# Optimization experiments

Measured on AMD Instinct MI355X. Metric: run time of the kernel, lower is better.

Reference implementation:

```python
import jax, jax.numpy as jnp
import numpy as np

N, IN_F, HID, HEADS, OUT = 50000, 128, 32, 4, 40
E = 800000
LN_EPS = 1e-5


def setup_inputs() -> dict:
    key = jax.random.key(0)
    ks = jax.random.split(key, 16)
    d1 = HEADS * HID  # 128
    s_in = 1.0 / np.sqrt(IN_F)
    s_d1 = 1.0 / np.sqrt(d1)
    return {
        "x": jax.random.normal(ks[0], (N, IN_F), jnp.float32),
        "edge_index": jax.random.randint(ks[1], (2, E), 0, N, jnp.int64),
        # layer 1 (GATv2, heads=4, concat=True)
        "Wl1": jax.random.normal(ks[2], (IN_F, d1), jnp.float32) * s_in,
        "bl1": jnp.zeros((d1,), jnp.float32),
        "Wr1": jax.random.normal(ks[3], (IN_F, d1), jnp.float32) * s_in,
        "br1": jnp.zeros((d1,), jnp.float32),
        "att1": jax.random.normal(ks[4], (HEADS, HID), jnp.float32) * s_d1,
        "b1": jnp.zeros((d1,), jnp.float32),
        # LayerNorm over hidden_channels*heads
        "g1": jnp.ones((d1,), jnp.float32),
        "be1": jnp.zeros((d1,), jnp.float32),
        # layer 2 (GATv2, heads=1, concat=False)
        "Wl2": jax.random.normal(ks[5], (d1, OUT), jnp.float32) * s_d1,
        "bl2": jnp.zeros((OUT,), jnp.float32),
        "Wr2": jax.random.normal(ks[6], (d1, OUT), jnp.float32) * s_d1,
        "br2": jnp.zeros((OUT,), jnp.float32),
        "att2": jax.random.normal(ks[7], (1, OUT), jnp.float32) / np.sqrt(OUT),
        "b2": jnp.zeros((OUT,), jnp.float32),
    }


def gatv2(x, src, tgt, Wl, bl, Wr, br, att, bias, heads, C, concat):
    n = x.shape[0]
    xl = (x @ Wl + bl).reshape(n, heads, C)  # source transform
    xr = (x @ Wr + br).reshape(n, heads, C)  # target transform
    h = xl[src] + xr[tgt]                    # [E,H,C]
    e = jnp.sum(jax.nn.leaky_relu(h, 0.2) * att, axis=-1)  # [E,H]
    # segment softmax over edges sharing the same target node
    m = jax.ops.segment_max(e, tgt, num_segments=n)        # [N,H]
    m = jnp.where(jnp.isfinite(m), m, 0.0)
    p = jnp.exp(e - m[tgt])
    s = jax.ops.segment_sum(p, tgt, num_segments=n)
    alpha = p / (s[tgt] + 1e-16)                           # [E,H]
    out = jax.ops.segment_sum(alpha[..., None] * xl[src], tgt, num_segments=n)  # [N,H,C]
    out = out.reshape(n, heads * C) if concat else out.mean(axis=1)
    return out + bias


def layer_norm(x, g, b):
    mu = x.mean(-1, keepdims=True)
    var = x.var(-1, keepdims=True)
    return (x - mu) * jax.lax.rsqrt(var + LN_EPS) * g + b


def reference(x, edge_index, Wl1, bl1, Wr1, br1, att1, b1, g1, be1,
              Wl2, bl2, Wr2, br2, att2, b2):
    src, tgt = edge_index[0], edge_index[1]
    h = gatv2(x, src, tgt, Wl1, bl1, Wr1, br1, att1, b1, HEADS, HID, True)
    h = jax.nn.elu(layer_norm(h, g1, be1))
    # dropout is identity in eval mode
    return gatv2(h, src, tgt, Wl2, bl2, Wr2, br2, att2, b2, 1, OUT, False)
```

## Files before the change

### kernel.cpp

```cpp
#include <hip/hip_runtime.h>
#include <hip/hip_bf16.h>
#include <math.h>

#define NN 50000
#define EE 800000
#define NB_SCAN 49

typedef __attribute__((ext_vector_type(8))) short bf16x8;
typedef __attribute__((ext_vector_type(4))) float f32x4;
typedef __attribute__((ext_vector_type(2))) float f32x2;
typedef __attribute__((ext_vector_type(8))) unsigned short ushortx8;

#define OFF_XBF  ((size_t)0)
#define SZ_XBF   ((size_t)NN * 128 * 2)
#define OFF_XL1B (OFF_XBF + SZ_XBF)
#define SZ_XL1B  ((size_t)NN * 128 * 2)
#define OFF_XR1  (OFF_XL1B + SZ_XL1B)
#define SZ_XR1   ((size_t)NN * 128 * 4)
#define OFF_H1B  (OFF_XR1 + SZ_XR1)
#define SZ_H1B   ((size_t)NN * 128 * 2)
#define OFF_XL2B (OFF_H1B + SZ_H1B)
#define SZ_XL2B  ((size_t)NN * 40 * 2)
#define OFF_XR2  (OFF_XL2B + SZ_XL2B)
#define SZ_XR2   ((size_t)NN * 40 * 4)
#define OFF_BP1  (OFF_XR2 + SZ_XR2)
#define SZ_BP1   ((size_t)32768 * 2)
#define OFF_BP2  (OFF_BP1 + SZ_BP1)
#define SZ_BP2   ((size_t)10240 * 2)
#define OFF_BB1  (OFF_BP2 + SZ_BP2)
#define SZ_BB1   ((size_t)1024)
#define OFF_BB2  (OFF_BB1 + SZ_BB1)
#define SZ_BB2   ((size_t)512)
#define OFF_DEG  (OFF_BB2 + SZ_BB2)
#define SZ_DEG   ((size_t)NN * 4)
#define OFF_OFFS (OFF_DEG + SZ_DEG)
#define SZ_OFFS  ((size_t)200192)
#define OFF_CUR  (OFF_OFFS + SZ_OFFS)
#define SZ_CUR   ((size_t)NN * 4)
#define OFF_CSR  (OFF_CUR + SZ_CUR)
#define SZ_CSR   ((size_t)EE * 4)
#define OFF_BSUM (OFF_CSR + SZ_CSR)
#define SZ_BSUM  ((size_t)256)

__device__ __forceinline__ unsigned short f2bf(float f) {
    union { float f; unsigned u; } v;
    v.f = f;
    unsigned r = v.u + 0x7fffu + ((v.u >> 16) & 1u);
    return (unsigned short)(r >> 16);
}
__device__ __forceinline__ f32x2 bf2f2(unsigned u) {
    union { unsigned u; float f; } lo, hi;
    lo.u = u << 16;
    hi.u = u & 0xffff0000u;
    f32x2 r;
    r.x = lo.f;
    r.y = hi.f;
    return r;
}

__device__ __forceinline__ f32x2 pk_add(f32x2 a, f32x2 b) {
    f32x2 d;
    asm("v_pk_add_f32 %0, %1, %2" : "=v"(d) : "v"(a), "v"(b));
    return d;
}
__device__ __forceinline__ f32x2 pk_mul(f32x2 a, f32x2 b) {
    f32x2 d;
    asm("v_pk_mul_f32 %0, %1, %2" : "=v"(d) : "v"(a), "v"(b));
    return d;
}
__device__ __forceinline__ f32x2 pk_fma(f32x2 a, f32x2 b, f32x2 c) {
    f32x2 d;
    asm("v_pk_fma_f32 %0, %1, %2, %3" : "=v"(d) : "v"(a), "v"(b), "v"(c));
    return d;
}
__device__ __forceinline__ f32x2 pk_abs2(f32x2 a) {
    f32x2 r;
    r.x = __builtin_fabsf(a.x);
    r.y = __builtin_fabsf(a.y);
    return r;
}

#define DPP_ADD(t, ctrl) \
    ((t) + __int_as_float(__builtin_amdgcn_mov_dpp(__float_as_int(t), (ctrl), 0xF, 0xF, true)))

__global__ void prep_kernel(
    const float* __restrict__ x, unsigned short* __restrict__ XBF,
    const float* __restrict__ Wl1, const float* __restrict__ bl1,
    const float* __restrict__ Wr1, const float* __restrict__ br1,
    const float* __restrict__ Wl2, const float* __restrict__ bl2,
    const float* __restrict__ Wr2, const float* __restrict__ br2,
    unsigned short* __restrict__ BP1, float* __restrict__ BB1,
    unsigned short* __restrict__ BP2, float* __restrict__ BB2,
    int* __restrict__ DEG) {
    int i = blockIdx.x * blockDim.x + threadIdx.x;
    if (i < NN * 128 / 8) {
        const float4* p = (const float4*)x + (size_t)i * 2;
        float4 v0 = p[0], v1 = p[1];
        ushortx8 o;
        o[0] = f2bf(v0.x); o[1] = f2bf(v0.y); o[2] = f2bf(v0.z); o[3] = f2bf(v0.w);
        o[4] = f2bf(v1.x); o[5] = f2bf(v1.y); o[6] = f2bf(v1.z); o[7] = f2bf(v1.w);
        *((ushortx8*)XBF + i) = o;
    }
    if (i < NN) DEG[i] = 0;
    if (i < 32768) {
        int j = i & 7, l = (i >> 3) & 63, nt = (i >> 9) & 15, kt = i >> 13;
        int k = kt * 32 + ((l >> 4) << 3) + j;
        int n = nt * 16 + (l & 15);
        float v = (n < 128) ? Wl1[k * 128 + n] : Wr1[k * 128 + (n - 128)];
        BP1[i] = f2bf(v);
    }
    if (i < 10240) {
        int j = i & 7, l = (i >> 3) & 63;
        int rest = i >> 9;
        int nt = rest % 5, kt = rest / 5;
        int k = kt * 32 + ((l >> 4) << 3) + j;
        int n = nt * 16 + (l & 15);
        float v = (n < 40) ? Wl2[k * 40 + n] : Wr2[k * 40 + (n - 40)];
        BP2[i] = f2bf(v);
    }
    if (i < 256) BB1[i] = (i < 128) ? bl1[i] : br1[i - 128];
    if (i < 80) BB2[i] = (i < 40) ? bl2[i] : br2[i - 40];
}

__global__ void hist_kernel(const int* __restrict__ tgts, int* __restrict__ deg, int e_) {
    int e = blockIdx.x * blockDim.x + threadIdx.x;
    if (e < e_) atomicAdd(&deg[tgts[e]], 1);
}

__global__ __launch_bounds__(1024) void scan_bsum_kernel(
    const int* __restrict__ deg, int* __restrict__ bsum, int n) {
    __shared__ int ws[16];
    int lane = threadIdx.x & 63, w = threadIdx.x >> 6;
    int i = blockIdx.x * 1024 + threadIdx.x;
    int v = (i < n) ? deg[i] : 0;
#pragma unroll
    for (int d = 32; d >= 1; d >>= 1) v += __shfl_xor(v, d, 64);
    if (lane == 0) ws[w] = v;
    __syncthreads();
    if (threadIdx.x < 16) {
        int xv = ws[threadIdx.x];
#pragma unroll
        for (int d = 8; d >= 1; d >>= 1) xv += __shfl_xor(xv, d, 16);
        if (threadIdx.x == 0) bsum[blockIdx.x] = xv;
    }
}

__global__ __launch_bounds__(1024) void scan_final_kernel(
    const int* __restrict__ deg, const int* __restrict__ bsum,
    int* __restrict__ off, int* __restrict__ cur, int n) {
    __shared__ int wsum[16];
    __shared__ int carrySh;
    int lane = threadIdx.x & 63, w = threadIdx.x >> 6;
    if (threadIdx.x < 64) {
        int v = ((int)threadIdx.x < (int)blockIdx.x) ? bsum[threadIdx.x] : 0;
#pragma unroll
        for (int d = 32; d >= 1; d >>= 1) v += __shfl_xor(v, d, 64);
        if (threadIdx.x == 0) carrySh = v;
    }
    int i = blockIdx.x * 1024 + threadIdx.x;
    int v = (i < n) ? deg[i] : 0;
    int incl = v;
#pragma unroll
    for (int d = 1; d < 64; d <<= 1) {
        int t = __shfl_up(incl, d, 64);
        if (lane >= d) incl += t;
    }
    if (lane == 63) wsum[w] = incl;
    __syncthreads();
    if (threadIdx.x < 16) {
        int xv = wsum[threadIdx.x];
#pragma unroll
        for (int d = 1; d < 16; d <<= 1) {
            int t = __shfl_up(xv, d, 16);
            if ((int)threadIdx.x >= d) xv += t;
        }
        wsum[threadIdx.x] = xv;
    }
    __syncthreads();
    int add = (w > 0) ? wsum[w - 1] : 0;
    int carry = carrySh;
    if (i < n) {
        int tot = carry + incl + add;
        off[i + 1] = tot;
        cur[i] = tot - v;
    }
    if (i == 0) off[0] = 0;
}

__global__ void scatter_kernel(const int* __restrict__ srcs, const int* __restrict__ tgts,
                               int* __restrict__ cur, int* __restrict__ csr, int e_) {
    int e = blockIdx.x * blockDim.x + threadIdx.x;
    if (e < e_) {
        int t = tgts[e];
        int pos = atomicAdd(&cur[t], 1);
        csr[pos] = srcs[e];
    }
}

__global__ __launch_bounds__(256) void gemm_mfma_kernel(
    const unsigned short* __restrict__ Abf, const unsigned short* __restrict__ BP,
    const float* __restrict__ bias, unsigned short* __restrict__ Cbf,
    float* __restrict__ Cf, int M, int NT, int NSPLIT) {
    int wave = (blockIdx.x * blockDim.x + threadIdx.x) >> 6;
    int lane = threadIdx.x & 63;
    int r0 = wave * 16;
    if (r0 >= M) return;
    int koff = (lane >> 4) << 3;
    const unsigned short* ap = &Abf[(size_t)(r0 + (lane & 15)) * 128 + koff];
    bf16x8 a0 = *(const bf16x8*)(ap);
    bf16x8 a1 = *(const bf16x8*)(ap + 32);
    bf16x8 a2 = *(const bf16x8*)(ap + 64);
    bf16x8 a3 = *(const bf16x8*)(ap + 96);
    int NR = (NT << 4) - NSPLIT;
    int col = lane & 15;
    int rb = r0 + ((lane >> 4) << 2);
    size_t ktStride = (size_t)NT * 512;
    for (int nt = 0; nt < NT; ++nt) {
        const unsigned short* bp = &BP[((size_t)nt * 64 + lane) * 8];
        f32x4 acc = {0.f, 0.f, 0.f, 0.f};
        acc = __builtin_amdgcn_mfma_f32_16x16x32_bf16(a0, *(const bf16x8*)(bp), acc, 0, 0, 0);
        acc = __builtin_amdgcn_mfma_f32_16x16x32_bf16(a1, *(const bf16x8*)(bp + ktStride), acc, 0, 0, 0);
        acc = __builtin_amdgcn_mfma_f32_16x16x32_bf16(a2, *(const bf16x8*)(bp + 2 * ktStride), acc, 0, 0, 0);
        acc = __builtin_amdgcn_mfma_f32_16x16x32_bf16(a3, *(const bf16x8*)(bp + 3 * ktStride), acc, 0, 0, 0);
        int c = (nt << 4) + col;
        float bb = bias[c];
        if (c < NSPLIT) {
#pragma unroll
            for (int j = 0; j < 4; ++j) Cbf[(size_t)(rb + j) * NSPLIT + c] = f2bf(acc[j] + bb);
        } else {
#pragma unroll
            for (int j = 0; j < 4; ++j) Cf[(size_t)(rb + j) * NR + (c - NSPLIT)] = acc[j] + bb;
        }
    }
}

__global__ __launch_bounds__(256) void gat_edge1_kernel(
    const unsigned short* __restrict__ XL1B, const float* __restrict__ XR1,
    const int* __restrict__ off, const int* __restrict__ csr,
    const float* __restrict__ att, const float* __restrict__ b1,
    const float* __restrict__ g1, const float* __restrict__ be1,
    unsigned short* __restrict__ H1B) {
    int wid = threadIdx.x >> 6;
    int lane = threadIdx.x & 63;
    int node = blockIdx.x * 4 + wid;
    if (node >= NN) return;
    int grp = lane >> 4;
    int sub = lane & 15;
    int cbase = sub << 3;
    const float* xrrow = &XR1[(size_t)node * 128];
    float4 xrA = *(const float4*)&xrrow[cbase];
    float4 xrB = *(const float4*)&xrrow[cbase + 4];
    float4 atA = *(const float4*)&att[cbase];
    float4 atB = *(const float4*)&att[cbase + 4];
    f32x2 xr01 = {xrA.x, xrA.y}, xr23 = {xrA.z, xrA.w};
    f32x2 xr45 = {xrB.x, xrB.y}, xr67 = {xrB.z, xrB.w};
    f32x2 at01 = {atA.x, atA.y}, at23 = {atA.z, atA.w};
    f32x2 at45 = {atB.x, atB.y}, at67 = {atB.z, atB.w};
    f32x2 c06 = {0.6f, 0.6f}, c04 = {0.4f, 0.4f};
    f32x2 acc01 = {0.f, 0.f}, acc23 = {0.f, 0.f}, acc45 = {0.f, 0.f}, acc67 = {0.f, 0.f};
    float s = 0.f;
    int jb = off[node], je = off[node + 1];
    int deg = je - jb;

    auto process = [&](uint4 q, int eo) {
        f32x2 xl01 = bf2f2(q.x), xl23 = bf2f2(q.y), xl45 = bf2f2(q.z), xl67 = bf2f2(q.w);
        f32x2 h01 = pk_add(xl01, xr01);
        f32x2 h23 = pk_add(xl23, xr23);
        f32x2 h45 = pk_add(xl45, xr45);
        f32x2 h67 = pk_add(xl67, xr67);
        f32x2 u01 = pk_fma(pk_abs2(h01), c04, pk_mul(h01, c06));
        f32x2 u23 = pk_fma(pk_abs2(h23), c04, pk_mul(h23, c06));
        f32x2 u45 = pk_fma(pk_abs2(h45), c04, pk_mul(h45, c06));
        f32x2 u67 = pk_fma(pk_abs2(h67), c04, pk_mul(h67, c06));
        f32x2 t2 = pk_mul(u01, at01);
        t2 = pk_fma(u23, at23, t2);
        t2 = pk_fma(u45, at45, t2);
        t2 = pk_fma(u67, at67, t2);
        float t = t2.x + t2.y;
        t = DPP_ADD(t, 0xB1);
        t = DPP_ADD(t, 0x4E);
        t = (eo < deg) ? t : -1e30f;
        float p = __expf(t);
        f32x2 pp;
        pp.x = p;
        pp.y = p;
        acc01 = pk_fma(pp, xl01, acc01);
        acc23 = pk_fma(pp, xl23, acc23);
        acc45 = pk_fma(pp, xl45, acc45);
        acc67 = pk_fma(pp, xl67, acc67);
        s += p;
    };

    for (int ch = 0; ch < deg; ch += 16) {
        int sidx = csr[min(jb + ch + sub, je - 1)];
        int s0 = __shfl(sidx, grp, 16);
        int s1 = __shfl(sidx, 4 + grp, 16);
        int s2 = __shfl(sidx, 8 + grp, 16);
        int s3 = __shfl(sidx, 12 + grp, 16);
        uint4 q0 = *(const uint4*)&XL1B[(size_t)s0 * 128 + cbase];
        uint4 q1 = *(const uint4*)&XL1B[(size_t)s1 * 128 + cbase];
        uint4 q2 = *(const uint4*)&XL1B[(size_t)s2 * 128 + cbase];
        uint4 q3 = *(const uint4*)&XL1B[(size_t)s3 * 128 + cbase];
        process(q0, ch + grp);
        process(q1, ch + 4 + grp);
        process(q2, ch + 8 + grp);
        process(q3, ch + 12 + grp);
    }

    float a0 = acc01.x, a1 = acc01.y, a2 = acc23.x, a3 = acc23.y;
    float a4 = acc45.x, a5 = acc45.y, a6 = acc67.x, a7 = acc67.y;
#pragma unroll
    for (int d = 16; d <= 32; d <<= 1) {
        s += __shfl_xor(s, d, 64);
        a0 += __shfl_xor(a0, d, 64);
        a1 += __shfl_xor(a1, d, 64);
        a2 += __shfl_xor(a2, d, 64);
        a3 += __shfl_xor(a3, d, 64);
        a4 += __shfl_xor(a4, d, 64);
        a5 += __shfl_xor(a5, d, 64);
        a6 += __shfl_xor(a6, d, 64);
        a7 += __shfl_xor(a7, d, 64);
    }
    float inv = 1.f / (s + 1e-16f);
    float4 bA = *(const float4*)&b1[cbase];
    float4 bB = *(const float4*)&b1[cbase + 4];
    float o[8];
    o[0] = a0 * inv + bA.x;
    o[1] = a1 * inv + bA.y;
    o[2] = a2 * inv + bA.z;
    o[3] = a3 * inv + bA.w;
    o[4] = a4 * inv + bB.x;
    o[5] = a5 * inv + bB.y;
    o[6] = a6 * inv + bB.z;
    o[7] = a7 * inv + bB.w;
    float sum = 0.f, sq = 0.f;
#pragma unroll
    for (int j = 0; j < 8; ++j) {
        sum += o[j];
        sq = fmaf(o[j], o[j], sq);
    }
#pragma unroll
    for (int d = 1; d <= 8; d <<= 1) {
        sum += __shfl_xor(sum, d, 64);
        sq += __shfl_xor(sq, d, 64);
    }
    float mu = sum * (1.f / 128.f);
    float var = sq * (1.f / 128.f) - mu * mu;
    float rs = rsqrtf(var + 1e-5f);
    if (grp == 0) {
        float4 gA = *(const float4*)&g1[cbase];
        float4 gB = *(const float4*)&g1[cbase + 4];
        float4 eA = *(const float4*)&be1[cbase];
        float4 eB = *(const float4*)&be1[cbase + 4];
        float y[8];
        y[0] = (o[0] - mu) * rs * gA.x + eA.x;
        y[1] = (o[1] - mu) * rs * gA.y + eA.y;
        y[2] = (o[2] - mu) * rs * gA.z + eA.z;
        y[3] = (o[3] - mu) * rs * gA.w + eA.w;
        y[4] = (o[4] - mu) * rs * gB.x + eB.x;
        y[5] = (o[5] - mu) * rs * gB.y + eB.y;
        y[6] = (o[6] - mu) * rs * gB.z + eB.z;
        y[7] = (o[7] - mu) * rs * gB.w + eB.w;
        ushortx8 hw;
#pragma unroll
        for (int j = 0; j < 8; ++j) {
            float yy = y[j] > 0.f ? y[j] : expm1f(y[j]);
            hw[j] = f2bf(yy);
        }
        *(ushortx8*)&H1B[(size_t)node * 128 + cbase] = hw;
    }
}

__global__ __launch_bounds__(256) void gat_edge2_kernel(
    const unsigned short* __restrict__ XL2B, const float* __restrict__ XR2,
    const int* __restrict__ off, const int* __restrict__ csr,
    const float* __restrict__ att2, const float* __restrict__ b2,
    float* __restrict__ Y) {
    int wid = threadIdx.x >> 6;
    int lane = threadIdx.x & 63;
    int node = blockIdx.x * 4 + wid;
    if (node >= NN) return;
    int grp = lane >> 4;
    int sub = lane & 15;
    bool chact = sub < 10;
    int cbase = sub << 2;
    int cld = chact ? cbase : 0;
    float4 xr = make_float4(0.f, 0.f, 0.f, 0.f);
    float4 at = make_float4(0.f, 0.f, 0.f, 0.f);
    if (chact) {
        xr = *(const float4*)&XR2[(size_t)node * 40 + cbase];
        at = *(const float4*)&att2[cbase];
    }
    f32x2 xr01 = {xr.x, xr.y}, xr23 = {xr.z, xr.w};
    f32x2 at01 = {at.x, at.y}, at23 = {at.z, at.w};
    f32x2 c06 = {0.6f, 0.6f}, c04 = {0.4f, 0.4f};
    f32x2 acc01 = {0.f, 0.f}, acc23 = {0.f, 0.f};
    float s = 0.f;
    int jb = off[node], je = off[node + 1];
    int deg = je - jb;

    auto process = [&](uint2 q, int eo) {
        f32x2 xl01 = bf2f2(q.x), xl23 = bf2f2(q.y);
        f32x2 h01 = pk_add(xl01, xr01);
        f32x2 h23 = pk_add(xl23, xr23);
        f32x2 u01 = pk_fma(pk_abs2(h01), c04, pk_mul(h01, c06));
        f32x2 u23 = pk_fma(pk_abs2(h23), c04, pk_mul(h23, c06));
        f32x2 t2 = pk_mul(u01, at01);
        t2 = pk_fma(u23, at23, t2);
        float t = t2.x + t2.y;
        t = DPP_ADD(t, 0xB1);
        t = DPP_ADD(t, 0x4E);
        t = DPP_ADD(t, 0x124);
        t = DPP_ADD(t, 0x128);
        t = (eo < deg) ? t : -1e30f;
        float p = __expf(t);
        f32x2 pp;
        pp.x = p;
        pp.y = p;
        acc01 = pk_fma(pp, xl01, acc01);
        acc23 = pk_fma(pp, xl23, acc23);
        s += p;
    };

    for (int ch = 0; ch < deg; ch += 16) {
        int sidx = csr[min(jb + ch + sub, je - 1)];
        int s0 = __shfl(sidx, grp, 16);
        int s1 = __shfl(sidx, 4 + grp, 16);
        int s2 = __shfl(sidx, 8 + grp, 16);
        int s3 = __shfl(sidx, 12 + grp, 16);
        uint2 q0 = *(const uint2*)&XL2B[(size_t)s0 * 40 + cld];
        uint2 q1 = *(const uint2*)&XL2B[(size_t)s1 * 40 + cld];
        uint2 q2 = *(const uint2*)&XL2B[(size_t)s2 * 40 + cld];
        uint2 q3 = *(const uint2*)&XL2B[(size_t)s3 * 40 + cld];
        process(q0, ch + grp);
        process(q1, ch + 4 + grp);
        process(q2, ch + 8 + grp);
        process(q3, ch + 12 + grp);
    }

    float a0 = acc01.x, a1 = acc01.y, a2 = acc23.x, a3 = acc23.y;
#pragma unroll
    for (int d = 16; d <= 32; d <<= 1) {
        s += __shfl_xor(s, d, 64);
        a0 += __shfl_xor(a0, d, 64);
        a1 += __shfl_xor(a1, d, 64);
        a2 += __shfl_xor(a2, d, 64);
        a3 += __shfl_xor(a3, d, 64);
    }
    if (grp == 0 && chact) {
        float inv = 1.f / (s + 1e-16f);
        float4 bb = *(const float4*)&b2[cbase];
        float4 y;
        y.x = a0 * inv + bb.x;
        y.y = a1 * inv + bb.y;
        y.z = a2 * inv + bb.z;
        y.w = a3 * inv + bb.w;
        *(float4*)&Y[(size_t)node * 40 + cbase] = y;
    }
}

extern "C" void kernel_launch(void* const* d_in, const int* in_sizes, int n_in,
                              void* d_out, int out_size, void* d_ws, size_t ws_size,
                              hipStream_t stream) {
    const float* x = (const float*)d_in[0];
    const int* ei = (const int*)d_in[1];
    const float* Wl1 = (const float*)d_in[2];
    const float* bl1 = (const float*)d_in[3];
    const float* Wr1 = (const float*)d_in[4];
    const float* br1 = (const float*)d_in[5];
    const float* att1 = (const float*)d_in[6];
    const float* b1 = (const float*)d_in[7];
    const float* g1 = (const float*)d_in[8];
    const float* be1 = (const float*)d_in[9];
    const float* Wl2 = (const float*)d_in[10];
    const float* bl2 = (const float*)d_in[11];
    const float* Wr2 = (const float*)d_in[12];
    const float* br2 = (const float*)d_in[13];
    const float* att2 = (const float*)d_in[14];
    const float* b2 = (const float*)d_in[15];

    const int* srcs = ei;
    const int* tgts = ei + EE;

    char* ws = (char*)d_ws;
    unsigned short* XBF = (unsigned short*)(ws + OFF_XBF);
    unsigned short* XL1B = (unsigned short*)(ws + OFF_XL1B);
    float* XR1 = (float*)(ws + OFF_XR1);
    unsigned short* H1B = (unsigned short*)(ws + OFF_H1B);
    unsigned short* XL2B = (unsigned short*)(ws + OFF_XL2B);
    float* XR2 = (float*)(ws + OFF_XR2);
    unsigned short* BP1 = (unsigned short*)(ws + OFF_BP1);
    unsigned short* BP2 = (unsigned short*)(ws + OFF_BP2);
    float* BB1 = (float*)(ws + OFF_BB1);
    float* BB2 = (float*)(ws + OFF_BB2);
    int* DEG = (int*)(ws + OFF_DEG);
    int* OFFS = (int*)(ws + OFF_OFFS);
    int* CUR = (int*)(ws + OFF_CUR);
    int* CSR = (int*)(ws + OFF_CSR);
    int* BSUM = (int*)(ws + OFF_BSUM);

    float* Y = (float*)d_out;

    prep_kernel<<<(NN * 128 / 8 + 255) / 256, 256, 0, stream>>>(
        x, XBF, Wl1, bl1, Wr1, br1, Wl2, bl2, Wr2, br2, BP1, BB1, BP2, BB2, DEG);

    hist_kernel<<<(EE + 255) / 256, 256, 0, stream>>>(tgts, DEG, EE);
    scan_bsum_kernel<<<NB_SCAN, 1024, 0, stream>>>(DEG, BSUM, NN);
    scan_final_kernel<<<NB_SCAN, 1024, 0, stream>>>(DEG, BSUM, OFFS, CUR, NN);
    scatter_kernel<<<(EE + 255) / 256, 256, 0, stream>>>(srcs, tgts, CUR, CSR, EE);

    gemm_mfma_kernel<<<(3125 + 3) / 4, 256, 0, stream>>>(XBF, BP1, BB1, XL1B, XR1, NN, 16, 128);

    gat_edge1_kernel<<<(NN + 3) / 4, 256, 0, stream>>>(XL1B, XR1, OFFS, CSR, att1, b1, g1, be1, H1B);

    gemm_mfma_kernel<<<(3125 + 3) / 4, 256, 0, stream>>>(H1B, BP2, BB2, XL2B, XR2, NN, 5, 40);

    gat_edge2_kernel<<<(NN + 3) / 4, 256, 0, stream>>>(XL2B, XR2, OFFS, CSR, att2, b2, Y);
}
```

Measured before the change: 202.1 us.

## Split fused GAT edge kernels into edge-parallel score and per-head aggregation passes

Replaces each fused per-node GAT edge kernel with separate passes. An edge-parallel kernel computes exp(score) per edge and writes it to a buffer, a gather kernel aggregates (launched once per head for layer 1), and a separate LayerNorm+ELU kernel follows. The scatter now also stores each edge's target so the score pass can run one thread per edge. This is meant to balance load across edges regardless of node degree and to narrow each aggregation gather to one head. In exchange it adds extra global traffic for the score and pre-norm buffers, more launches, and re-reads of XL1B four times.

```diff
diff --git a/kernel.cpp b/kernel.cpp
--- a/kernel.cpp
+++ b/kernel.cpp
@@ -8,39 +8,28 @@
 
 typedef __attribute__((ext_vector_type(8))) short bf16x8;
 typedef __attribute__((ext_vector_type(4))) float f32x4;
-typedef __attribute__((ext_vector_type(2))) float f32x2;
 typedef __attribute__((ext_vector_type(8))) unsigned short ushortx8;
 
-#define OFF_XBF  ((size_t)0)
-#define SZ_XBF   ((size_t)NN * 128 * 2)
-#define OFF_XL1B (OFF_XBF + SZ_XBF)
-#define SZ_XL1B  ((size_t)NN * 128 * 2)
-#define OFF_XR1  (OFF_XL1B + SZ_XL1B)
-#define SZ_XR1   ((size_t)NN * 128 * 4)
-#define OFF_H1B  (OFF_XR1 + SZ_XR1)
-#define SZ_H1B   ((size_t)NN * 128 * 2)
-#define OFF_XL2B (OFF_H1B + SZ_H1B)
-#define SZ_XL2B  ((size_t)NN * 40 * 2)
-#define OFF_XR2  (OFF_XL2B + SZ_XL2B)
-#define SZ_XR2   ((size_t)NN * 40 * 4)
-#define OFF_BP1  (OFF_XR2 + SZ_XR2)
-#define SZ_BP1   ((size_t)32768 * 2)
-#define OFF_BP2  (OFF_BP1 + SZ_BP1)
-#define SZ_BP2   ((size_t)10240 * 2)
-#define OFF_BB1  (OFF_BP2 + SZ_BP2)
-#define SZ_BB1   ((size_t)1024)
-#define OFF_BB2  (OFF_BB1 + SZ_BB1)
-#define SZ_BB2   ((size_t)512)
-#define OFF_DEG  (OFF_BB2 + SZ_BB2)
-#define SZ_DEG   ((size_t)NN * 4)
-#define OFF_OFFS (OFF_DEG + SZ_DEG)
-#define SZ_OFFS  ((size_t)200192)
-#define OFF_CUR  (OFF_OFFS + SZ_OFFS)
-#define SZ_CUR   ((size_t)NN * 4)
-#define OFF_CSR  (OFF_CUR + SZ_CUR)
-#define SZ_CSR   ((size_t)EE * 4)
-#define OFF_BSUM (OFF_CSR + SZ_CSR)
-#define SZ_BSUM  ((size_t)256)
+#define OFF_XBF   ((size_t)0)
+#define OFF_P1    ((size_t)0)
+#define OFF_XL2B  ((size_t)0)
+#define OFF_XR2   ((size_t)4000000)
+#define OFF_XL1B  ((size_t)12800000)
+#define OFF_H1B   ((size_t)12800000)
+#define OFF_XR1   ((size_t)25600000)
+#define OFF_H1PRE ((size_t)25600000)
+#define OFF_P2    ((size_t)51200000)
+#define OFF_S1    ((size_t)54400000)
+#define OFF_BP1   ((size_t)55200000)
+#define OFF_BP2   ((size_t)55265536)
+#define OFF_BB1   ((size_t)55286016)
+#define OFF_BB2   ((size_t)55287040)
+#define OFF_DEG   ((size_t)55287552)
+#define OFF_OFFS  ((size_t)55487552)
+#define OFF_CUR   ((size_t)55687808)
+#define OFF_BSUM  ((size_t)55887808)
+#define OFF_CSR   ((size_t)55888064)
+#define OFF_CTG   ((size_t)59088064)
 
 __device__ __forceinline__ unsigned short f2bf(float f) {
     union { float f; unsigned u; } v;
@@ -48,40 +37,17 @@
     unsigned r = v.u + 0x7fffu + ((v.u >> 16) & 1u);
     return (unsigned short)(r >> 16);
 }
-__device__ __forceinline__ f32x2 bf2f2(unsigned u) {
-    union { unsigned u; float f; } lo, hi;
-    lo.u = u << 16;
-    hi.u = u & 0xffff0000u;
-    f32x2 r;
-    r.x = lo.f;
-    r.y = hi.f;
-    return r;
-}
-
-__device__ __forceinline__ f32x2 pk_add(f32x2 a, f32x2 b) {
-    f32x2 d;
-    asm("v_pk_add_f32 %0, %1, %2" : "=v"(d) : "v"(a), "v"(b));
-    return d;
-}
-__device__ __forceinline__ f32x2 pk_mul(f32x2 a, f32x2 b) {
-    f32x2 d;
-    asm("v_pk_mul_f32 %0, %1, %2" : "=v"(d) : "v"(a), "v"(b));
-    return d;
-}
-__device__ __forceinline__ f32x2 pk_fma(f32x2 a, f32x2 b, f32x2 c) {
-    f32x2 d;
-    asm("v_pk_fma_f32 %0, %1, %2, %3" : "=v"(d) : "v"(a), "v"(b), "v"(c));
-    return d;
-}
-__device__ __forceinline__ f32x2 pk_abs2(f32x2 a) {
-    f32x2 r;
-    r.x = __builtin_fabsf(a.x);
-    r.y = __builtin_fabsf(a.y);
-    return r;
-}
-
-#define DPP_ADD(t, ctrl) \
-    ((t) + __int_as_float(__builtin_amdgcn_mov_dpp(__float_as_int(t), (ctrl), 0xF, 0xF, true)))
+__device__ __forceinline__ float bfl(unsigned u) {
+    union { unsigned u; float f; } v;
+    v.u = u << 16;
+    return v.f;
+}
+__device__ __forceinline__ float bfh(unsigned u) {
+    union { unsigned u; float f; } v;
+    v.u = u & 0xffff0000u;
+    return v.f;
+}
+__device__ __forceinline__ float lrelu02(float h) { return fmaxf(h, 0.2f * h); }
 
 __global__ void prep_kernel(
     const float* __restrict__ x, unsigned short* __restrict__ XBF,
@@ -188,12 +154,14 @@
 }
 
 __global__ void scatter_kernel(const int* __restrict__ srcs, const int* __restrict__ tgts,
-                               int* __restrict__ cur, int* __restrict__ csr, int e_) {
+                               int* __restrict__ cur, int* __restrict__ csr,
+                               int* __restrict__ ctg, int e_) {
     int e = blockIdx.x * blockDim.x + threadIdx.x;
     if (e < e_) {
         int t = tgts[e];
         int pos = atomicAdd(&cur[t], 1);
         csr[pos] = srcs[e];
+        ctg[pos] = t;
     }
 }
 
@@ -234,61 +202,63 @@
     }
 }
 
-__global__ __launch_bounds__(256) void gat_edge1_kernel(
+__global__ __launch_bounds__(256) void score1_kernel(
     const unsigned short* __restrict__ XL1B, const float* __restrict__ XR1,
-    const int* __restrict__ off, const int* __restrict__ csr,
-    const float* __restrict__ att, const float* __restrict__ b1,
-    const float* __restrict__ g1, const float* __restrict__ be1,
-    unsigned short* __restrict__ H1B) {
+    const int* __restrict__ csr, const int* __restrict__ ctg,
+    const float* __restrict__ att, float* __restrict__ P1) {
+    int e = blockIdx.x * 256 + threadIdx.x;
+    int s = csr[e], t = ctg[e];
+    const uint4* xlp = (const uint4*)(XL1B + (size_t)s * 128);
+    const float* xr = XR1 + (size_t)t * 128;
+    float p4[4];
+#pragma unroll
+    for (int h = 0; h < 4; ++h) {
+        float acc = 0.f;
+#pragma unroll
+        for (int q = 0; q < 4; ++q) {
+            uint4 u = xlp[h * 4 + q];
+            int cb = h * 32 + q * 8;
+            float4 x0 = *(const float4*)&xr[cb];
+            float4 x1 = *(const float4*)&xr[cb + 4];
+            float4 a0 = *(const float4*)&att[cb];
+            float4 a1 = *(const float4*)&att[cb + 4];
+            acc = fmaf(lrelu02(bfl(u.x) + x0.x), a0.x, acc);
+            acc = fmaf(lrelu02(bfh(u.x) + x0.y), a0.y, acc);
+            acc = fmaf(lrelu02(bfl(u.y) + x0.z), a0.z, acc);
+            acc = fmaf(lrelu02(bfh(u.y) + x0.w), a0.w, acc);
+            acc = fmaf(lrelu02(bfl(u.z) + x1.x), a1.x, acc);
+            acc = fmaf(lrelu02(bfh(u.z) + x1.y), a1.y, acc);
+            acc = fmaf(lrelu02(bfl(u.w) + x1.z), a1.z, acc);
+            acc = fmaf(lrelu02(bfh(u.w) + x1.w), a1.w, acc);
+        }
+        p4[h] = __expf(acc);
+    }
+    *(float4*)&P1[(size_t)e * 4] = make_float4(p4[0], p4[1], p4[2], p4[3]);
+}
+
+__global__ __launch_bounds__(256) void agg1_kernel(
+    const unsigned short* __restrict__ XL1B, const int* __restrict__ off,
+    const int* __restrict__ csr, const float* __restrict__ P1,
+    float* __restrict__ H1pre, float* __restrict__ S1, int cb) {
     int wid = threadIdx.x >> 6;
     int lane = threadIdx.x & 63;
     int node = blockIdx.x * 4 + wid;
     if (node >= NN) return;
     int grp = lane >> 4;
     int sub = lane & 15;
-    int cbase = sub << 3;
-    const float* xrrow = &XR1[(size_t)node * 128];
-    float4 xrA = *(const float4*)&xrrow[cbase];
-    float4 xrB = *(const float4*)&xrrow[cbase + 4];
-    float4 atA = *(const float4*)&att[cbase];
-    float4 atB = *(const float4*)&att[cbase + 4];
-    f32x2 xr01 = {xrA.x, xrA.y}, xr23 = {xrA.z, xrA.w};
-    f32x2 xr45 = {xrB.x, xrB.y}, xr67 = {xrB.z, xrB.w};
-    f32x2 at01 = {atA.x, atA.y}, at23 = {atA.z, atA.w};
-    f32x2 at45 = {atB.x, atB.y}, at67 = {atB.z, atB.w};
-    f32x2 c06 = {0.6f, 0.6f}, c04 = {0.4f, 0.4f};
-    f32x2 acc01 = {0.f, 0.f}, acc23 = {0.f, 0.f}, acc45 = {0.f, 0.f}, acc67 = {0.f, 0.f};
-    float s = 0.f;
     int jb = off[node], je = off[node + 1];
     int deg = je - jb;
-
-    auto process = [&](uint4 q, int eo) {
-        f32x2 xl01 = bf2f2(q.x), xl23 = bf2f2(q.y), xl45 = bf2f2(q.z), xl67 = bf2f2(q.w);
-        f32x2 h01 = pk_add(xl01, xr01);
-        f32x2 h23 = pk_add(xl23, xr23);
-        f32x2 h45 = pk_add(xl45, xr45);
-        f32x2 h67 = pk_add(xl67, xr67);
-        f32x2 u01 = pk_fma(pk_abs2(h01), c04, pk_mul(h01, c06));
-        f32x2 u23 = pk_fma(pk_abs2(h23), c04, pk_mul(h23, c06));
-        f32x2 u45 = pk_fma(pk_abs2(h45), c04, pk_mul(h45, c06));
-        f32x2 u67 = pk_fma(pk_abs2(h67), c04, pk_mul(h67, c06));
-        f32x2 t2 = pk_mul(u01, at01);
-        t2 = pk_fma(u23, at23, t2);
-        t2 = pk_fma(u45, at45, t2);
-        t2 = pk_fma(u67, at67, t2);
-        float t = t2.x + t2.y;
-        t = DPP_ADD(t, 0xB1);
-        t = DPP_ADD(t, 0x4E);
-        t = (eo < deg) ? t : -1e30f;
-        float p = __expf(t);
-        f32x2 pp;
-        pp.x = p;
-        pp.y = p;
-        acc01 = pk_fma(pp, xl01, acc01);
-        acc23 = pk_fma(pp, xl23, acc23);
-        acc45 = pk_fma(pp, xl45, acc45);
-        acc67 = pk_fma(pp, xl67, acc67);
-        s += p;
+    const unsigned short* base = XL1B + cb * 32 + sub * 2;
+    float a0 = 0.f, a1 = 0.f, sl = 0.f;
+
+    auto proc = [&](int srcv, int eo) {
+        unsigned u = *(const unsigned*)(base + (size_t)srcv * 128);
+        int eidx = jb + eo;
+        float p = P1[(size_t)min(eidx, je - 1) * 4 + cb];
+        p = (eo < deg) ? p : 0.f;
+        a0 = fmaf(p, bfl(u), a0);
+        a1 = fmaf(p, bfh(u), a1);
+        sl += p;
     };
 
     for (int ch = 0; ch < deg; ch += 16) {
@@ -297,85 +267,90 @@
         int s1 = __shfl(sidx, 4 + grp, 16);
         int s2 = __shfl(sidx, 8 + grp, 16);
         int s3 = __shfl(sidx, 12 + grp, 16);
-        uint4 q0 = *(const uint4*)&XL1B[(size_t)s0 * 128 + cbase];
-        uint4 q1 = *(const uint4*)&XL1B[(size_t)s1 * 128 + cbase];
-        uint4 q2 = *(const uint4*)&XL1B[(size_t)s2 * 128 + cbase];
-        uint4 q3 = *(const uint4*)&XL1B[(size_t)s3 * 128 + cbase];
-        process(q0, ch + grp);
-        process(q1, ch + 4 + grp);
-        process(q2, ch + 8 + grp);
-        process(q3, ch + 12 + grp);
-    }
-
-    float a0 = acc01.x, a1 = acc01.y, a2 = acc23.x, a3 = acc23.y;
-    float a4 = acc45.x, a5 = acc45.y, a6 = acc67.x, a7 = acc67.y;
+        proc(s0, ch + grp);
+        proc(s1, ch + 4 + grp);
+        proc(s2, ch + 8 + grp);
+        proc(s3, ch + 12 + grp);
+    }
 #pragma unroll
     for (int d = 16; d <= 32; d <<= 1) {
-        s += __shfl_xor(s, d, 64);
         a0 += __shfl_xor(a0, d, 64);
         a1 += __shfl_xor(a1, d, 64);
-        a2 += __shfl_xor(a2, d, 64);
-        a3 += __shfl_xor(a3, d, 64);
-        a4 += __shfl_xor(a4, d, 64);
-        a5 += __shfl_xor(a5, d, 64);
-        a6 += __shfl_xor(a6, d, 64);
-        a7 += __shfl_xor(a7, d, 64);
-    }
-    float inv = 1.f / (s + 1e-16f);
-    float4 bA = *(const float4*)&b1[cbase];
-    float4 bB = *(const float4*)&b1[cbase + 4];
-    float o[8];
-    o[0] = a0 * inv + bA.x;
-    o[1] = a1 * inv + bA.y;
-    o[2] = a2 * inv + bA.z;
-    o[3] = a3 * inv + bA.w;
-    o[4] = a4 * inv + bB.x;
-    o[5] = a5 * inv + bB.y;
-    o[6] = a6 * inv + bB.z;
-    o[7] = a7 * inv + bB.w;
-    float sum = 0.f, sq = 0.f;
-#pragma unroll
-    for (int j = 0; j < 8; ++j) {
-        sum += o[j];
-        sq = fmaf(o[j], o[j], sq);
-    }
-#pragma unroll
-    for (int d = 1; d <= 8; d <<= 1) {
+        sl += __shfl_xor(sl, d, 64);
+    }
+    if (grp == 0) {
+        float2 v;
+        v.x = a0;
+        v.y = a1;
+        *(float2*)&H1pre[(size_t)node * 128 + cb * 32 + sub * 2] = v;
+        if (sub == 0) S1[node * 4 + cb] = sl;
+    }
+}
+
+__global__ __launch_bounds__(256) void ln1_kernel(
+    const float* __restrict__ H1pre, const float* __restrict__ S1,
+    const float* __restrict__ b1, const float* __restrict__ g1,
+    const float* __restrict__ be1, unsigned short* __restrict__ H1B) {
+    int wid = threadIdx.x >> 6;
+    int lane = threadIdx.x & 63;
+    int node = blockIdx.x * 4 + wid;
+    if (node >= NN) return;
+    int c = lane * 2;
+    float2 v = *(const float2*)&H1pre[(size_t)node * 128 + c];
+    float sl = S1[node * 4 + (lane >> 4)];
+    float inv = 1.f / (sl + 1e-16f);
+    float o0 = v.x * inv + b1[c];
+    float o1 = v.y * inv + b1[c + 1];
+    float sum = o0 + o1, sq = o0 * o0 + o1 * o1;
+#pragma unroll
+    for (int d = 32; d >= 1; d >>= 1) {
         sum += __shfl_xor(sum, d, 64);
         sq += __shfl_xor(sq, d, 64);
     }
     float mu = sum * (1.f / 128.f);
     float var = sq * (1.f / 128.f) - mu * mu;
     float rs = rsqrtf(var + 1e-5f);
-    if (grp == 0) {
-        float4 gA = *(const float4*)&g1[cbase];
-        float4 gB = *(const float4*)&g1[cbase + 4];
-        float4 eA = *(const float4*)&be1[cbase];
-        float4 eB = *(const float4*)&be1[cbase + 4];
-        float y[8];
-        y[0] = (o[0] - mu) * rs * gA.x + eA.x;
-        y[1] = (o[1] - mu) * rs * gA.y + eA.y;
-        y[2] = (o[2] - mu) * rs * gA.z + eA.z;
-        y[3] = (o[3] - mu) * rs * gA.w + eA.w;
-        y[4] = (o[4] - mu) * rs * gB.x + eB.x;
-        y[5] = (o[5] - mu) * rs * gB.y + eB.y;
-        y[6] = (o[6] - mu) * rs * gB.z + eB.z;
-        y[7] = (o[7] - mu) * rs * gB.w + eB.w;
-        ushortx8 hw;
-#pragma unroll
-        for (int j = 0; j < 8; ++j) {
-            float yy = y[j] > 0.f ? y[j] : expm1f(y[j]);
-            hw[j] = f2bf(yy);
-        }
-        *(ushortx8*)&H1B[(size_t)node * 128 + cbase] = hw;
-    }
-}
-
-__global__ __launch_bounds__(256) void gat_edge2_kernel(
+    float y0 = (o0 - mu) * rs * g1[c] + be1[c];
+    float y1 = (o1 - mu) * rs * g1[c + 1] + be1[c + 1];
+    y0 = y0 > 0.f ? y0 : expm1f(y0);
+    y1 = y1 > 0.f ? y1 : expm1f(y1);
+    unsigned o = (unsigned)f2bf(y0) | ((unsigned)f2bf(y1) << 16);
+    ((unsigned*)H1B)[(size_t)node * 64 + lane] = o;
+}
+
+__global__ __launch_bounds__(256) void score2_kernel(
     const unsigned short* __restrict__ XL2B, const float* __restrict__ XR2,
-    const int* __restrict__ off, const int* __restrict__ csr,
-    const float* __restrict__ att2, const float* __restrict__ b2,
-    float* __restrict__ Y) {
+    const int* __restrict__ csr, const int* __restrict__ ctg,
+    const float* __restrict__ att2, float* __restrict__ P2) {
+    int e = blockIdx.x * 256 + threadIdx.x;
+    int s = csr[e], t = ctg[e];
+    const uint4* xlp = (const uint4*)(XL2B + (size_t)s * 40);
+    const float* xr = XR2 + (size_t)t * 40;
+    float acc = 0.f;
+#pragma unroll
+    for (int q = 0; q < 5; ++q) {
+        uint4 u = xlp[q];
+        int cb = q * 8;
+        float4 x0 = *(const float4*)&xr[cb];
+        float4 x1 = *(const float4*)&xr[cb + 4];
+        float4 a0 = *(const float4*)&att2[cb];
+        float4 a1 = *(const float4*)&att2[cb + 4];
+        acc = fmaf(lrelu02(bfl(u.x) + x0.x), a0.x, acc);
+        acc = fmaf(lrelu02(bfh(u.x) + x0.y), a0.y, acc);
+        acc = fmaf(lrelu02(bfl(u.y) + x0.z), a0.z, acc);
+        acc = fmaf(lrelu02(bfh(u.y) + x0.w), a0.w, acc);
+        acc = fmaf(lrelu02(bfl(u.z) + x1.x), a1.x, acc);
+        acc = fmaf(lrelu02(bfh(u.z) + x1.y), a1.y, acc);
+        acc = fmaf(lrelu02(bfl(u.w) + x1.z), a1.z, acc);
+        acc = fmaf(lrelu02(bfh(u.w) + x1.w), a1.w, acc);
+    }
+    P2[e] = __expf(acc);
+}
+
+__global__ __launch_bounds__(256) void agg2_kernel(
+    const unsigned short* __restrict__ XL2B, const int* __restrict__ off,
+    const int* __restrict__ csr, const float* __restrict__ P2,
+    const float* __restrict__ b2, float* __restrict__ Y) {
     int wid = threadIdx.x >> 6;
     int lane = threadIdx.x & 63;
     int node = blockIdx.x * 4 + wid;
@@ -383,43 +358,20 @@
     int grp = lane >> 4;
     int sub = lane & 15;
     bool chact = sub < 10;
-    int cbase = sub << 2;
-    int cld = chact ? cbase : 0;
-    float4 xr = make_float4(0.f, 0.f, 0.f, 0.f);
-    float4 at = make_float4(0.f, 0.f, 0.f, 0.f);
-    if (chact) {
-        xr = *(const float4*)&XR2[(size_t)node * 40 + cbase];
-        at = *(const float4*)&att2[cbase];
-    }
-    f32x2 xr01 = {xr.x, xr.y}, xr23 = {xr.z, xr.w};
-    f32x2 at01 = {at.x, at.y}, at23 = {at.z, at.w};
-    f32x2 c06 = {0.6f, 0.6f}, c04 = {0.4f, 0.4f};
-    f32x2 acc01 = {0.f, 0.f}, acc23 = {0.f, 0.f};
-    float s = 0.f;
+    int cld = chact ? sub * 4 : 0;
     int jb = off[node], je = off[node + 1];
     int deg = je - jb;
-
-    auto process = [&](uint2 q, int eo) {
-        f32x2 xl01 = bf2f2(q.x), xl23 = bf2f2(q.y);
-        f32x2 h01 = pk_add(xl01, xr01);
-        f32x2 h23 = pk_add(xl23, xr23);
-        f32x2 u01 = pk_fma(pk_abs2(h01), c04, pk_mul(h01, c06));
-        f32x2 u23 = pk_fma(pk_abs2(h23), c04, pk_mul(h23, c06));
-        f32x2 t2 = pk_mul(u01, at01);
-        t2 = pk_fma(u23, at23, t2);
-        float t = t2.x + t2.y;
-        t = DPP_ADD(t, 0xB1);
-        t = DPP_ADD(t, 0x4E);
-        t = DPP_ADD(t, 0x124);
-        t = DPP_ADD(t, 0x128);
-        t = (eo < deg) ? t : -1e30f;
-        float p = __expf(t);
-        f32x2 pp;
-        pp.x = p;
-        pp.y = p;
-        acc01 = pk_fma(pp, xl01, acc01);
-        acc23 = pk_fma(pp, xl23, acc23);
-        s += p;
+    float a0 = 0.f, a1 = 0.f, a2 = 0.f, a3 = 0.f, sl = 0.f;
+
+    auto proc = [&](int srcv, int eo) {
+        uint2 u = *(const uint2*)(XL2B + (size_t)srcv * 40 + cld);
+        float p = P2[min(jb + eo, je - 1)];
+        p = (eo < deg) ? p : 0.f;
+        a0 = fmaf(p, bfl(u.x), a0);
+        a1 = fmaf(p, bfh(u.x), a1);
+        a2 = fmaf(p, bfl(u.y), a2);
+        a3 = fmaf(p, bfh(u.y), a3);
+        sl += p;
     };
 
     for (int ch = 0; ch < deg; ch += 16) {
@@ -428,34 +380,28 @@
         int s1 = __shfl(sidx, 4 + grp, 16);
         int s2 = __shfl(sidx, 8 + grp, 16);
         int s3 = __shfl(sidx, 12 + grp, 16);
-        uint2 q0 = *(const uint2*)&XL2B[(size_t)s0 * 40 + cld];
-        uint2 q1 = *(const uint2*)&XL2B[(size_t)s1 * 40 + cld];
-        uint2 q2 = *(const uint2*)&XL2B[(size_t)s2 * 40 + cld];
-        uint2 q3 = *(const uint2*)&XL2B[(size_t)s3 * 40 + cld];
-        process(q0, ch + grp);
-        process(q1, ch + 4 + grp);
-        process(q2, ch + 8 + grp);
-        process(q3, ch + 12 + grp);
-    }
-
-    float a0 = acc01.x, a1 = acc01.y, a2 = acc23.x, a3 = acc23.y;
+        proc(s0, ch + grp);
+        proc(s1, ch + 4 + grp);
+        proc(s2, ch + 8 + grp);
+        proc(s3, ch + 12 + grp);
+    }
 #pragma unroll
     for (int d = 16; d <= 32; d <<= 1) {
-        s += __shfl_xor(s, d, 64);
         a0 += __shfl_xor(a0, d, 64);
         a1 += __shfl_xor(a1, d, 64);
         a2 += __shfl_xor(a2, d, 64);
         a3 += __shfl_xor(a3, d, 64);
+        sl += __shfl_xor(sl, d, 64);
     }
     if (grp == 0 && chact) {
-        float inv = 1.f / (s + 1e-16f);
-        float4 bb = *(const float4*)&b2[cbase];
+        float inv = 1.f / (sl + 1e-16f);
+        int c = sub * 4;
         float4 y;
-        y.x = a0 * inv + bb.x;
-        y.y = a1 * inv + bb.y;
-        y.z = a2 * inv + bb.z;
-        y.w = a3 * inv + bb.w;
-        *(float4*)&Y[(size_t)node * 40 + cbase] = y;
+        y.x = a0 * inv + b2[c];
+        y.y = a1 * inv + b2[c + 1];
+        y.z = a2 * inv + b2[c + 2];
+        y.w = a3 * inv + b2[c + 3];
+        *(float4*)&Y[(size_t)node * 40 + c] = y;
     }
 }
 
@@ -484,11 +430,15 @@
 
     char* ws = (char*)d_ws;
     unsigned short* XBF = (unsigned short*)(ws + OFF_XBF);
-    unsigned short* XL1B = (unsigned short*)(ws + OFF_XL1B);
-    float* XR1 = (float*)(ws + OFF_XR1);
-    unsigned short* H1B = (unsigned short*)(ws + OFF_H1B);
+    float* P1 = (float*)(ws + OFF_P1);
     unsigned short* XL2B = (unsigned short*)(ws + OFF_XL2B);
     float* XR2 = (float*)(ws + OFF_XR2);
+    unsigned short* XL1B = (unsigned short*)(ws + OFF_XL1B);
+    unsigned short* H1B = (unsigned short*)(ws + OFF_H1B);
+    float* XR1 = (float*)(ws + OFF_XR1);
+    float* H1pre = (float*)(ws + OFF_H1PRE);
+    float* P2 = (float*)(ws + OFF_P2);
+    float* S1 = (float*)(ws + OFF_S1);
     unsigned short* BP1 = (unsigned short*)(ws + OFF_BP1);
     unsigned short* BP2 = (unsigned short*)(ws + OFF_BP2);
     float* BB1 = (float*)(ws + OFF_BB1);
@@ -497,6 +447,7 @@
     int* OFFS = (int*)(ws + OFF_OFFS);
     int* CUR = (int*)(ws + OFF_CUR);
     int* CSR = (int*)(ws + OFF_CSR);
+    int* CTG = (int*)(ws + OFF_CTG);
     int* BSUM = (int*)(ws + OFF_BSUM);
 
     float* Y = (float*)d_out;
@@ -507,13 +458,20 @@
     hist_kernel<<<(EE + 255) / 256, 256, 0, stream>>>(tgts, DEG, EE);
     scan_bsum_kernel<<<NB_SCAN, 1024, 0, stream>>>(DEG, BSUM, NN);
     scan_final_kernel<<<NB_SCAN, 1024, 0, stream>>>(DEG, BSUM, OFFS, CUR, NN);
-    scatter_kernel<<<(EE + 255) / 256, 256, 0, stream>>>(srcs, tgts, CUR, CSR, EE);
+    scatter_kernel<<<(EE + 255) / 256, 256, 0, stream>>>(srcs, tgts, CUR, CSR, CTG, EE);
 
     gemm_mfma_kernel<<<(3125 + 3) / 4, 256, 0, stream>>>(XBF, BP1, BB1, XL1B, XR1, NN, 16, 128);
 
-    gat_edge1_kernel<<<(NN + 3) / 4, 256, 0, stream>>>(XL1B, XR1, OFFS, CSR, att1, b1, g1, be1, H1B);
+    score1_kernel<<<3125, 256, 0, stream>>>(XL1B, XR1, CSR, CTG, att1, P1);
+
+    for (int cb = 0; cb < 4; ++cb)
+        agg1_kernel<<<12500, 256, 0, stream>>>(XL1B, OFFS, CSR, P1, H1pre, S1, cb);
+
+    ln1_kernel<<<12500, 256, 0, stream>>>(H1pre, S1, b1, g1, be1, H1B);
 
     gemm_mfma_kernel<<<(3125 + 3) / 4, 256, 0, stream>>>(H1B, BP2, BB2, XL2B, XR2, NN, 5, 40);
 
-    gat_edge2_kernel<<<(NN + 3) / 4, 256, 0, stream>>>(XL2B, XR2, OFFS, CSR, att2, b2, Y);
-}
+    score2_kernel<<<3125, 256, 0, stream>>>(XL2B, XR2, CSR, CTG, att2, P2);
+
+    agg2_kernel<<<12500, 256, 0, stream>>>(XL2B, OFFS, CSR, P2, b2, Y);
+}
```

Result: slower. 297.5 us (+47.2%).
